# Kernel optimization log

Hardware: AMD Instinct MI355X
Metric: run time of the kernel (lower is better)

Reference implementation:

```python
import jax, jax.numpy as jnp
import numpy as np

N = 50000      # nodes
E = 1600000    # edges (avg degree 32)
F_IN = 256     # input feature dim
H = 128        # hidden == output size of GCN
C = 40         # num_class


def setup_inputs() -> dict:
    key = jax.random.key(0)
    ks = jax.random.split(key, 13)
    inp = {
        "features": jax.random.normal(ks[0], (N, F_IN), dtype=jnp.float32),
        "src": jax.random.randint(ks[1], (E,), 0, N, dtype=jnp.int32),
        "dst": jax.random.randint(ks[2], (E,), 0, N, dtype=jnp.int32),
        "edge_weight": jax.random.uniform(ks[3], (E,), dtype=jnp.float32),
        "y": jax.random.normal(ks[4], (N, C), dtype=jnp.float32),
        # GCN layer 1
        "W1": jax.random.normal(ks[5], (F_IN, H), dtype=jnp.float32) / np.sqrt(F_IN),
        "b1": jnp.zeros((H,), dtype=jnp.float32),
        # GCN layer 2
        "W2": jax.random.normal(ks[6], (H, H), dtype=jnp.float32) / np.sqrt(H),
        "b2": jnp.zeros((H,), dtype=jnp.float32),
        # y_fc_emb: Linear(num_class, output_size)
        "We": jax.random.normal(ks[7], (C, H), dtype=jnp.float32) / np.sqrt(C),
        "be": jnp.zeros((H,), dtype=jnp.float32),
        # y_fc: Linear(hidden*2, num_class)
        "Wf": jax.random.normal(ks[8], (2 * H, C), dtype=jnp.float32) / np.sqrt(2 * H),
        "bf": jnp.zeros((C,), dtype=jnp.float32),
    }
    return inp


def _spmm(edge_weight, src, dst, x, n):
    # (sparse adj) @ x : out[i] = sum_{(j->i)} w_ji * x[j]
    return jax.ops.segment_sum(edge_weight[:, None] * x[src], dst, num_segments=n)


def reference(features, src, dst, edge_weight, y, W1, b1, W2, b2, We, be, Wf, bf):
    n = features.shape[0]
    # F.normalize: L2 row-normalize with eps=1e-12 clamp
    norm = jnp.maximum(jnp.linalg.norm(features, axis=1, keepdims=True), 1e-12)
    x = features / norm
    # GCN layer 1: relu(adj @ (x @ W1) + b1)   (dropout = 0)
    h = jax.nn.relu(_spmm(edge_weight, src, dst, x @ W1, n) + b1)
    # GCN layer 2: adj @ (h @ W2) + b2
    h = _spmm(edge_weight, src, dst, h @ W2, n) + b2
    # label embedding + head
    y_emb = y @ We + be
    logits = jnp.concatenate([y_emb, h], axis=1) @ Wf + bf
    return jax.nn.softmax(logits, axis=-1)
```

## Files before the change

### kernel.cpp

```cpp
#include <hip/hip_runtime.h>
#include <hip/hip_bf16.h>
#include <hip/hip_fp16.h>
#include <cstdint>
#include <cstddef>
#include <cmath>

#define F_IN 256
#define HDIM 128
#define CCLS 40
#define NBMAX 1024
#define EPB_H 16384

typedef short bf16x8 __attribute__((ext_vector_type(8)));
typedef float f32x4 __attribute__((ext_vector_type(4)));

__device__ inline unsigned pkbf(float a, float b) {
  __hip_bfloat162 h = __float22bfloat162_rn(make_float2(a, b));
  unsigned u;
  __builtin_memcpy(&u, &h, 4);
  return u;
}
__device__ inline unsigned short bfr(float f) {
  __hip_bfloat16 h = __float2bfloat16(f);
  unsigned short u;
  __builtin_memcpy(&u, &h, 2);
  return u;
}
__device__ inline float f16tof(unsigned short hb) {
  __half hv;
  __builtin_memcpy(&hv, &hb, 2);
  return __half2float(hv);
}
__device__ inline unsigned short ftof16(float f) {
  __half hv = __float2half(f);
  unsigned short u;
  __builtin_memcpy(&u, &hv, 2);
  return u;
}

__global__ __launch_bounds__(256) void prep_kernel(const float* __restrict__ W1,
                                                   const float* __restrict__ W2,
                                                   unsigned short* __restrict__ W1T,
                                                   unsigned short* __restrict__ W2T,
                                                   const float* __restrict__ We,
                                                   const float* __restrict__ be,
                                                   const float* __restrict__ Wf,
                                                   const float* __restrict__ bf,
                                                   float* __restrict__ Wc,
                                                   float* __restrict__ bc,
                                                   const int* __restrict__ dst,
                                                   int* __restrict__ gcount,
                                                   int e, int nb) {
  const int b = blockIdx.x;
  const int t = threadIdx.x;
  if (b < 192) {
    int idx = b * 256 + t;
    if (idx < 128 * 256) {
      int nr = idx >> 8, k = idx & 255;
      W1T[idx] = bfr(W1[k * 128 + nr]);
    } else {
      int i2 = idx - 128 * 256;
      if (i2 < 128 * 128) {
        int nr = i2 >> 7, k = i2 & 127;
        W2T[i2] = bfr(W2[k * 128 + nr]);
      }
    }
  } else if (b < 194) {
    int part = b - 192;
    int lo = part * 800, hi = lo + 800;
    for (int i = lo + t; i < hi; i += 256) {
      int c = i / CCLS, j = i % CCLS;
      float s = 0.f;
      for (int f = 0; f < HDIM; ++f) s += We[c * HDIM + f] * Wf[f * CCLS + j];
      Wc[i] = s;
    }
    if (part == 0 && t < CCLS) {
      float s = bf[t];
      for (int f = 0; f < HDIM; ++f) s += be[f] * Wf[f * CCLS + t];
      bc[t] = s;
    }
  } else {
    __shared__ int h[NBMAX];
    for (int i = t; i < nb; i += 256) h[i] = 0;
    __syncthreads();
    int b4 = (b - 194) * (EPB_H / 4);
#pragma unroll
    for (int k = 0; k < EPB_H / 1024; ++k) {
      int gi = b4 + k * 256 + t;
      int e0 = gi * 4;
      int4 d = make_int4(-1, -1, -1, -1);
      if (e0 + 3 < e) d = ((const int4*)dst)[gi];
      else if (e0 < e) {
        d.x = dst[e0];
        if (e0 + 1 < e) d.y = dst[e0 + 1];
        if (e0 + 2 < e) d.z = dst[e0 + 2];
      }
      if (d.x >= 0) atomicAdd(&h[d.x >> 6], 1);
      if (d.y >= 0) atomicAdd(&h[d.y >> 6], 1);
      if (d.z >= 0) atomicAdd(&h[d.z >> 6], 1);
      if (d.w >= 0) atomicAdd(&h[d.w >> 6], 1);
    }
    __syncthreads();
    for (int i = t; i < nb; i += 256)
      if (h[i]) atomicAdd(&gcount[i], h[i]);
  }
}

#define EPB 8192
__global__ __launch_bounds__(256) void scatter_gemm1(const int* __restrict__ src,
                                                     const int* __restrict__ dst,
                                                     const float* __restrict__ w,
                                                     const int* __restrict__ gcount,
                                                     int* __restrict__ gcursor,
                                                     uint2* __restrict__ ews,
                                                     const float* __restrict__ X,
                                                     const unsigned short* __restrict__ WT,
                                                     unsigned short* __restrict__ C,
                                                     int e, int nb, int nsb, int M) {
  __shared__ char smem[64 * 264 * 2];
  const int t = threadIdx.x;
  if ((int)blockIdx.x < nsb) {
    int* hist = (int*)smem;
    int* sb   = hist + NBMAX;
    int* lcur = sb + NBMAX;
    int* part = lcur + NBMAX;
    for (int i = t; i < nb; i += 256) { hist[i] = 0; lcur[i] = 0; }
    __syncthreads();
    const int b4 = blockIdx.x * 2048;
    int4 dv[8];
#pragma unroll
    for (int k = 0; k < 8; ++k) {
      int gi = b4 + k * 256 + t;
      int e0 = gi * 4;
      int4 d = make_int4(-1, -1, -1, -1);
      if (e0 + 3 < e) d = ((const int4*)dst)[gi];
      else if (e0 < e) {
        d.x = dst[e0];
        if (e0 + 1 < e) d.y = dst[e0 + 1];
        if (e0 + 2 < e) d.z = dst[e0 + 2];
      }
      dv[k] = d;
      if (d.x >= 0) atomicAdd(&hist[d.x >> 6], 1);
      if (d.y >= 0) atomicAdd(&hist[d.y >> 6], 1);
      if (d.z >= 0) atomicAdd(&hist[d.z >> 6], 1);
      if (d.w >= 0) atomicAdd(&hist[d.w >> 6], 1);
    }
    __syncthreads();
    int v[4];
    int s = 0;
#pragma unroll
    for (int k = 0; k < 4; ++k) {
      int i = t * 4 + k;
      v[k] = (i < nb) ? gcount[i] : 0;
      s += v[k];
    }
    part[t] = s;
    __syncthreads();
    for (int off = 1; off < 256; off <<= 1) {
      int x = part[t];
      if (t >= off) x += part[t - off];
      __syncthreads();
      part[t] = x;
      __syncthreads();
    }
    int run = (t == 0) ? 0 : part[t - 1];
#pragma unroll
    for (int k = 0; k < 4; ++k) {
      int i = t * 4 + k;
      if (i < nb) sb[i] = run;
      run += v[k];
    }
    __syncthreads();
    for (int i = t; i < nb; i += 256) {
      int c = hist[i];
      sb[i] = sb[i] + (c ? atomicAdd(&gcursor[i], c) : 0);
    }
    __syncthreads();
#pragma unroll
    for (int k = 0; k < 8; ++k) {
      int gi = b4 + k * 256 + t;
      int e0 = gi * 4;
      if (e0 >= e) continue;
      int4 s4 = make_int4(0, 0, 0, 0);
      float4 w4 = make_float4(0.f, 0.f, 0.f, 0.f);
      if (e0 + 3 < e) { s4 = ((const int4*)src)[gi]; w4 = ((const float4*)w)[gi]; }
      else {
        s4.x = src[e0]; w4.x = w[e0];
        if (e0 + 1 < e) { s4.y = src[e0 + 1]; w4.y = w[e0 + 1]; }
        if (e0 + 2 < e) { s4.z = src[e0 + 2]; w4.z = w[e0 + 2]; }
      }
      int4 d = dv[k];
      if (d.x >= 0) { int bb = d.x >> 6; int r = atomicAdd(&lcur[bb], 1);
        ews[sb[bb] + r] = make_uint2(((unsigned)(d.x & 63) << 26) | (unsigned)s4.x, __float_as_uint(w4.x)); }
      if (d.y >= 0) { int bb = d.y >> 6; int r = atomicAdd(&lcur[bb], 1);
        ews[sb[bb] + r] = make_uint2(((unsigned)(d.y & 63) << 26) | (unsigned)s4.y, __float_as_uint(w4.y)); }
      if (d.z >= 0) { int bb = d.z >> 6; int r = atomicAdd(&lcur[bb], 1);
        ews[sb[bb] + r] = make_uint2(((unsigned)(d.z & 63) << 26) | (unsigned)s4.z, __float_as_uint(w4.z)); }
      if (d.w >= 0) { int bb = d.w >> 6; int r = atomicAdd(&lcur[bb], 1);
        ews[sb[bb] + r] = make_uint2(((unsigned)(d.w & 63) << 26) | (unsigned)s4.w, __float_as_uint(w4.w)); }
    }
  } else {
    unsigned short (*As)[264] = (unsigned short(*)[264])smem;
    const int w8 = t >> 6, l = t & 63;
    const int bm0 = (blockIdx.x - nsb) * 64;

    for (int rr = 0; rr < 16; ++rr) {
      int row = w8 * 16 + rr;
      int grow = bm0 + row;
      const float* p = X + (size_t)(grow < M ? grow : (M - 1)) * F_IN + l * 4;
      float4 v = *(const float4*)p;
      float s = v.x * v.x + v.y * v.y + v.z * v.z + v.w * v.w;
#pragma unroll
      for (int off = 32; off; off >>= 1) s += __shfl_xor(s, off, 64);
      float inv = 1.0f / fmaxf(sqrtf(s), 1e-12f);
      *(uint2*)&As[row][l * 4] =
          make_uint2(pkbf(v.x * inv, v.y * inv), pkbf(v.z * inv, v.w * inv));
    }

    const int ln = l & 15, quad = l >> 4;
    const int m0 = bm0 + w8 * 16;
    f32x4 acc[8];
#pragma unroll
    for (int i = 0; i < 8; ++i) acc[i] = (f32x4){0.f, 0.f, 0.f, 0.f};

#pragma unroll
    for (int k0 = 0; k0 < F_IN; k0 += 32) {
      bf16x8 af = *(const bf16x8*)&As[w8 * 16 + ln][k0 + quad * 8];
#pragma unroll
      for (int ti = 0; ti < 8; ++ti) {
        bf16x8 bfv = *(const bf16x8*)(WT + (size_t)(ti * 16 + ln) * F_IN + k0 + quad * 8);
        acc[ti] = __builtin_amdgcn_mfma_f32_16x16x32_bf16(af, bfv, acc[ti], 0, 0, 0);
      }
    }

#pragma unroll
    for (int r = 0; r < 4; ++r) {
      int grow = m0 + quad * 4 + r;
      if (grow < M) {
        unsigned short* cp = C + (size_t)grow * HDIM + ln;
#pragma unroll
        for (int ti = 0; ti < 8; ++ti) cp[ti * 16] = bfr(acc[ti][r]);
      }
    }
  }
}

__global__ __launch_bounds__(256) void bucket_sort(const uint2* __restrict__ ews,
                                                   const int* __restrict__ gcount,
                                                   unsigned* __restrict__ ews2,
                                                   int* __restrict__ row_off,
                                                   int n, int nb) {
  __shared__ int cnt64[64];
  __shared__ int cur[64];
  __shared__ int sred[4];
  const int t = threadIdx.x;
  const int b = blockIdx.x;
  int partial = 0;
  for (int i = t; i < b; i += 256) partial += gcount[i];
#pragma unroll
  for (int off = 32; off; off >>= 1) partial += __shfl_xor(partial, off, 64);
  if ((t & 63) == 0) sred[t >> 6] = partial;
  if (t < 64) cnt64[t] = 0;
  __syncthreads();
  const int e0 = sred[0] + sred[1] + sred[2] + sred[3];
  const int e1 = e0 + gcount[b];
  for (int i = e0 + t; i < e1; i += 256) atomicAdd(&cnt64[(unsigned)ews[i].x >> 26], 1);
  __syncthreads();
  if (t == 0) {
    int run = 0;
    for (int d = 0; d < 64; ++d) {
      int c = cnt64[d];
      cur[d] = run;
      run += c;
    }
  }
  __syncthreads();
  if (t < 64) {
    int node = b * 64 + t;
    if (node < n) row_off[node] = e0 + cur[t];
  }
  if (b == nb - 1 && t == 0) row_off[n] = e1;
  __syncthreads();
  for (int i = e0 + t; i < e1; i += 256) {
    uint2 p = ews[i];
    int d = (unsigned)p.x >> 26;
    int pos = e0 + atomicAdd(&cur[d], 1);
    unsigned rec = (p.x & 0xFFFFu) | ((unsigned)ftof16(__uint_as_float(p.y)) << 16);
    ews2[pos] = rec;
  }
}

#define SPMM_PAIR(ua, ub)                                                      \
  {                                                                            \
    unsigned u = half ? (ub) : (ua);                                           \
    float wt = f16tof((unsigned short)(u >> 16));                              \
    const uint2 xv = *(const uint2*)(xin + (size_t)(u & 0xFFFFu) * HDIM + fo); \
    acc.x = fmaf(wt, __uint_as_float(xv.x << 16), acc.x);                      \
    acc.y = fmaf(wt, __uint_as_float(xv.x & 0xFFFF0000u), acc.y);              \
    acc.z = fmaf(wt, __uint_as_float(xv.y << 16), acc.z);                      \
    acc.w = fmaf(wt, __uint_as_float(xv.y & 0xFFFF0000u), acc.w);              \
  }

template <int OUT_BF16>
__global__ __launch_bounds__(256) void spmm_bf16(const unsigned short* __restrict__ xin,
                                                 const unsigned* __restrict__ ews,
                                                 const int* __restrict__ row_off,
                                                 const float* __restrict__ bias,
                                                 void* __restrict__ outp, int n,
                                                 int do_relu) {
  const int t = threadIdx.x;
  const int l = t & 63;
  const int node = blockIdx.x * 4 + (t >> 6);
  if (node >= n) return;
  const int ue0 = __builtin_amdgcn_readfirstlane(row_off[node]);
  const int ue1 = __builtin_amdgcn_readfirstlane(row_off[node + 1]);
  const int cnt = ue1 - ue0;
  const unsigned* ep = ews + ue0;
  const int fo = (l & 31) * 4;
  const int half = l >> 5;
  float4 acc = make_float4(0.f, 0.f, 0.f, 0.f);

  int k = 0;
  for (; k + 16 <= cnt; k += 16) {
    unsigned a0 = ep[k + 0], a1 = ep[k + 1], a2 = ep[k + 2], a3 = ep[k + 3];
    unsigned a4 = ep[k + 4], a5 = ep[k + 5], a6 = ep[k + 6], a7 = ep[k + 7];
    unsigned a8 = ep[k + 8], a9 = ep[k + 9], a10 = ep[k + 10], a11 = ep[k + 11];
    unsigned a12 = ep[k + 12], a13 = ep[k + 13], a14 = ep[k + 14], a15 = ep[k + 15];
    SPMM_PAIR(a0, a1);
    SPMM_PAIR(a2, a3);
    SPMM_PAIR(a4, a5);
    SPMM_PAIR(a6, a7);
    SPMM_PAIR(a8, a9);
    SPMM_PAIR(a10, a11);
    SPMM_PAIR(a12, a13);
    SPMM_PAIR(a14, a15);
  }
  for (; k + 8 <= cnt; k += 8) {
    unsigned a0 = ep[k + 0], a1 = ep[k + 1], a2 = ep[k + 2], a3 = ep[k + 3];
    unsigned a4 = ep[k + 4], a5 = ep[k + 5], a6 = ep[k + 6], a7 = ep[k + 7];
    SPMM_PAIR(a0, a1);
    SPMM_PAIR(a2, a3);
    SPMM_PAIR(a4, a5);
    SPMM_PAIR(a6, a7);
  }
  for (; k < cnt; k += 2) {
    unsigned a0 = ep[k];
    unsigned a1 = (k + 1 < cnt) ? ep[k + 1] : 0u;
    SPMM_PAIR(a0, a1);
  }

  acc.x += __shfl_xor(acc.x, 32, 64);
  acc.y += __shfl_xor(acc.y, 32, 64);
  acc.z += __shfl_xor(acc.z, 32, 64);
  acc.w += __shfl_xor(acc.w, 32, 64);
  if (l < 32) {
    float4 bv = *(const float4*)(bias + fo);
    float4 r = make_float4(acc.x + bv.x, acc.y + bv.y, acc.z + bv.z, acc.w + bv.w);
    if (do_relu) {
      r.x = fmaxf(r.x, 0.f); r.y = fmaxf(r.y, 0.f);
      r.z = fmaxf(r.z, 0.f); r.w = fmaxf(r.w, 0.f);
    }
    if (OUT_BF16) {
      uint2 o = make_uint2(pkbf(r.x, r.y), pkbf(r.z, r.w));
      *(uint2*)((unsigned short*)outp + (size_t)node * HDIM + fo) = o;
    } else {
      *(float4*)((float*)outp + (size_t)node * HDIM + fo) = r;
    }
  }
}

template <int K>
__global__ __launch_bounds__(256) void gemm_mfma(const unsigned short* __restrict__ A,
                                                 const unsigned short* __restrict__ WT,
                                                 unsigned short* __restrict__ C, int M) {
  const int t = threadIdx.x;
  const int w = t >> 6, l = t & 63;
  const int ln = l & 15, quad = l >> 4;
  const int m0 = blockIdx.x * 64 + w * 16;
  const int arow = m0 + ln;
  const unsigned short* aptr = A + (size_t)(arow < M ? arow : (M - 1)) * K + quad * 8;

  f32x4 acc[8];
#pragma unroll
  for (int i = 0; i < 8; ++i) acc[i] = (f32x4){0.f, 0.f, 0.f, 0.f};

#pragma unroll
  for (int k0 = 0; k0 < K; k0 += 32) {
    bf16x8 af = *(const bf16x8*)(aptr + k0);
#pragma unroll
    for (int ti = 0; ti < 8; ++ti) {
      bf16x8 bfv = *(const bf16x8*)(WT + (size_t)(ti * 16 + ln) * K + k0 + quad * 8);
      acc[ti] = __builtin_amdgcn_mfma_f32_16x16x32_bf16(af, bfv, acc[ti], 0, 0, 0);
    }
  }

#pragma unroll
  for (int r = 0; r < 4; ++r) {
    int grow = m0 + quad * 4 + r;
    if (grow < M) {
      unsigned short* cp = C + (size_t)grow * HDIM + ln;
#pragma unroll
      for (int ti = 0; ti < 8; ++ti) cp[ti * 16] = bfr(acc[ti][r]);
    }
  }
}

__global__ __launch_bounds__(256) void head_kernel(const float* __restrict__ y,
                                                   const float* __restrict__ h2,
                                                   const float* __restrict__ Wc,
                                                   const float* __restrict__ bc,
                                                   const float* __restrict__ Wf,
                                                   float* __restrict__ out, int n) {
  __shared__ float sW[169 * CCLS];
  const int t = threadIdx.x;
  for (int i = t; i < 400; i += 256) ((float4*)sW)[i] = ((const float4*)Wc)[i];
  for (int i = t; i < 1280; i += 256)
    ((float4*)(sW + CCLS * CCLS))[i] = ((const float4*)(Wf + HDIM * CCLS))[i];
  if (t < 10) ((float4*)(sW + 168 * CCLS))[t] = ((const float4*)bc)[t];
  __syncthreads();

  const int node = blockIdx.x * 256 + t;
  const int nc = node < n ? node : n - 1;
  const float* zy = y + (size_t)nc * CCLS;
  const float* zh = h2 + (size_t)nc * HDIM;

  float acc[40];
#pragma unroll
  for (int cq = 0; cq < 10; ++cq) {
    float4 b4 = *(const float4*)&sW[168 * CCLS + cq * 4];
    acc[cq * 4 + 0] = b4.x; acc[cq * 4 + 1] = b4.y;
    acc[cq * 4 + 2] = b4.z; acc[cq * 4 + 3] = b4.w;
  }

#pragma unroll 2
  for (int kc = 0; kc < 10; ++kc) {
    float4 zv = *(const float4*)(zy + kc * 4);
    float zj[4] = {zv.x, zv.y, zv.z, zv.w};
#pragma unroll
    for (int j = 0; j < 4; ++j) {
      const float* wr = sW + (kc * 4 + j) * CCLS;
#pragma unroll
      for (int cq = 0; cq < 10; ++cq) {
        float4 w4 = *(const float4*)(wr + cq * 4);
        acc[cq * 4 + 0] = fmaf(zj[j], w4.x, acc[cq * 4 + 0]);
        acc[cq * 4 + 1] = fmaf(zj[j], w4.y, acc[cq * 4 + 1]);
        acc[cq * 4 + 2] = fmaf(zj[j], w4.z, acc[cq * 4 + 2]);
        acc[cq * 4 + 3] = fmaf(zj[j], w4.w, acc[cq * 4 + 3]);
      }
    }
  }
#pragma unroll 2
  for (int kc = 0; kc < 32; ++kc) {
    float4 zv = *(const float4*)(zh + kc * 4);
    float zj[4] = {zv.x, zv.y, zv.z, zv.w};
#pragma unroll
    for (int j = 0; j < 4; ++j) {
      const float* wr = sW + (40 + kc * 4 + j) * CCLS;
#pragma unroll
      for (int cq = 0; cq < 10; ++cq) {
        float4 w4 = *(const float4*)(wr + cq * 4);
        acc[cq * 4 + 0] = fmaf(zj[j], w4.x, acc[cq * 4 + 0]);
        acc[cq * 4 + 1] = fmaf(zj[j], w4.y, acc[cq * 4 + 1]);
        acc[cq * 4 + 2] = fmaf(zj[j], w4.z, acc[cq * 4 + 2]);
        acc[cq * 4 + 3] = fmaf(zj[j], w4.w, acc[cq * 4 + 3]);
      }
    }
  }

  float m = acc[0];
#pragma unroll
  for (int c = 1; c < 40; ++c) m = fmaxf(m, acc[c]);
  float sum = 0.f;
#pragma unroll
  for (int c = 0; c < 40; ++c) { acc[c] = __expf(acc[c] - m); sum += acc[c]; }
  float inv = 1.0f / sum;
  if (node < n) {
    float* op = out + (size_t)node * CCLS;
#pragma unroll
    for (int cq = 0; cq < 10; ++cq) {
      float4 o = make_float4(acc[cq * 4 + 0] * inv, acc[cq * 4 + 1] * inv,
                             acc[cq * 4 + 2] * inv, acc[cq * 4 + 3] * inv);
      *(float4*)(op + cq * 4) = o;
    }
  }
}

extern "C" void kernel_launch(void* const* d_in, const int* in_sizes, int n_in,
                              void* d_out, int out_size, void* d_ws, size_t ws_size,
                              hipStream_t stream) {
  (void)n_in; (void)out_size; (void)ws_size;
  const float* features = (const float*)d_in[0];
  const int*   src      = (const int*)d_in[1];
  const int*   dst      = (const int*)d_in[2];
  const float* ew       = (const float*)d_in[3];
  const float* y        = (const float*)d_in[4];
  const float* W1       = (const float*)d_in[5];
  const float* b1       = (const float*)d_in[6];
  const float* W2       = (const float*)d_in[7];
  const float* b2       = (const float*)d_in[8];
  const float* We       = (const float*)d_in[9];
  const float* be       = (const float*)d_in[10];
  const float* Wf       = (const float*)d_in[11];
  const float* bf       = (const float*)d_in[12];
  float* out = (float*)d_out;

  const int n = in_sizes[0] / F_IN;
  const int e = in_sizes[1];
  const int nb = (n + 63) >> 6;

  char* w = (char*)d_ws;
  auto take = [&](size_t bytes) {
    char* p = w;
    w += (bytes + 255) & ~(size_t)255;
    return p;
  };
  int*   gz       = (int*)take((size_t)2 * nb * 4);
  int*   gcount   = gz;
  int*   gcursor  = gz + nb;
  int*   row_off  = (int*)take((size_t)(n + 1) * 4);
  uint2* ews      = (uint2*)take((size_t)e * 8);
  unsigned* ews2  = (unsigned*)take((size_t)(e + 16) * 4);
  unsigned short* bufH1  = (unsigned short*)take((size_t)n * HDIM * 2);
  unsigned short* bufH2  = (unsigned short*)take((size_t)n * HDIM * 2);
  float* bufS     = (float*)take((size_t)n * HDIM * 4);
  unsigned short* W1T = (unsigned short*)take((size_t)HDIM * F_IN * 2);
  unsigned short* W2T = (unsigned short*)take((size_t)HDIM * HDIM * 2);
  float* Wc       = (float*)take(CCLS * CCLS * 4);
  float* bc       = (float*)take(CCLS * 4);

  const int hb = (e + EPB_H - 1) / EPB_H;
  const int nsb = (e + EPB - 1) / EPB;
  const int ngb = (n + 63) / 64;
  hipMemsetAsync(gz, 0, (size_t)2 * nb * 4, stream);
  prep_kernel<<<194 + hb, 256, 0, stream>>>(W1, W2, W1T, W2T, We, be, Wf, bf, Wc, bc,
                                            dst, gcount, e, nb);
  scatter_gemm1<<<nsb + ngb, 256, 0, stream>>>(src, dst, ew, gcount, gcursor, ews,
                                               features, W1T, bufH1, e, nb, nsb, n);
  bucket_sort<<<nb, 256, 0, stream>>>(ews, gcount, ews2, row_off, n, nb);

  spmm_bf16<1><<<(n + 3) / 4, 256, 0, stream>>>(bufH1, ews2, row_off, b1, bufH2, n, 1);
  gemm_mfma<HDIM><<<(n + 63) / 64, 256, 0, stream>>>(bufH2, W2T, bufH1, n);
  spmm_bf16<0><<<(n + 3) / 4, 256, 0, stream>>>(bufH1, ews2, row_off, b2, bufS, n, 0);
  head_kernel<<<(n + 255) / 256, 256, 0, stream>>>(y, bufS, Wc, bc, Wf, out, n);
}
```

Before: 343.8 us.

## Replace two-pass bucket sort with per-node counting and direct CSR scatter

The prep kernel now also counts edges per destination node with global atomics. A new row_scan kernel builds row offsets and per-node cursors from those counts. The scatter then writes packed fp16-weight records straight into their CSR slot using per-node global atomics. This removes the 8-byte intermediate edge buffer, the block-level histogram and scan in the scatter, and the separate bucket_sort pass. In exchange it adds millions of contended global atomics on a 50k-entry array and gives non-deterministic edge order within each row.

```diff
diff --git a/kernel.cpp b/kernel.cpp
--- a/kernel.cpp
+++ b/kernel.cpp
@@ -49,6 +49,7 @@
                                                    float* __restrict__ Wc,
                                                    float* __restrict__ bc,
                                                    const int* __restrict__ dst,
+                                                   int* __restrict__ ncnt,
                                                    int* __restrict__ gcount,
                                                    int e, int nb) {
   const int b = blockIdx.x;
@@ -95,112 +96,88 @@
         if (e0 + 1 < e) d.y = dst[e0 + 1];
         if (e0 + 2 < e) d.z = dst[e0 + 2];
       }
-      if (d.x >= 0) atomicAdd(&h[d.x >> 6], 1);
-      if (d.y >= 0) atomicAdd(&h[d.y >> 6], 1);
-      if (d.z >= 0) atomicAdd(&h[d.z >> 6], 1);
-      if (d.w >= 0) atomicAdd(&h[d.w >> 6], 1);
+      if (d.x >= 0) { atomicAdd(&h[d.x >> 6], 1); atomicAdd(&ncnt[d.x], 1); }
+      if (d.y >= 0) { atomicAdd(&h[d.y >> 6], 1); atomicAdd(&ncnt[d.y], 1); }
+      if (d.z >= 0) { atomicAdd(&h[d.z >> 6], 1); atomicAdd(&ncnt[d.z], 1); }
+      if (d.w >= 0) { atomicAdd(&h[d.w >> 6], 1); atomicAdd(&ncnt[d.w], 1); }
     }
     __syncthreads();
     for (int i = t; i < nb; i += 256)
       if (h[i]) atomicAdd(&gcount[i], h[i]);
   }
+}
+
+__global__ __launch_bounds__(256) void row_scan(const int* __restrict__ gcount,
+                                                const int* __restrict__ ncnt,
+                                                int* __restrict__ row_off,
+                                                int* __restrict__ cur,
+                                                int n, int nb, int e) {
+  __shared__ int sred[4];
+  const int t = threadIdx.x;
+  const int b = blockIdx.x;
+  int partial = 0;
+  for (int i = t; i < b; i += 256) partial += gcount[i];
+#pragma unroll
+  for (int off = 32; off; off >>= 1) partial += __shfl_xor(partial, off, 64);
+  if ((t & 63) == 0) sred[t >> 6] = partial;
+  __syncthreads();
+  const int e0 = sred[0] + sred[1] + sred[2] + sred[3];
+  if (t < 64) {
+    int node = b * 64 + t;
+    int c = (node < n) ? ncnt[node] : 0;
+    int x = c;
+#pragma unroll
+    for (int off = 1; off < 64; off <<= 1) {
+      int y = __shfl_up(x, off, 64);
+      if (t >= off) x += y;
+    }
+    int base = e0 + x - c;
+    if (node < n) { row_off[node] = base; cur[node] = base; }
+  }
+  if (b == nb - 1 && t == 0) row_off[n] = e;
 }
 
 #define EPB 8192
 __global__ __launch_bounds__(256) void scatter_gemm1(const int* __restrict__ src,
                                                      const int* __restrict__ dst,
                                                      const float* __restrict__ w,
-                                                     const int* __restrict__ gcount,
-                                                     int* __restrict__ gcursor,
-                                                     uint2* __restrict__ ews,
+                                                     int* __restrict__ cur,
+                                                     unsigned* __restrict__ ews2,
                                                      const float* __restrict__ X,
                                                      const unsigned short* __restrict__ WT,
                                                      unsigned short* __restrict__ C,
-                                                     int e, int nb, int nsb, int M) {
-  __shared__ char smem[64 * 264 * 2];
+                                                     int e, int nsb, int M) {
+  __shared__ unsigned short As[64][264];
   const int t = threadIdx.x;
   if ((int)blockIdx.x < nsb) {
-    int* hist = (int*)smem;
-    int* sb   = hist + NBMAX;
-    int* lcur = sb + NBMAX;
-    int* part = lcur + NBMAX;
-    for (int i = t; i < nb; i += 256) { hist[i] = 0; lcur[i] = 0; }
-    __syncthreads();
     const int b4 = blockIdx.x * 2048;
-    int4 dv[8];
-#pragma unroll
-    for (int k = 0; k < 8; ++k) {
-      int gi = b4 + k * 256 + t;
-      int e0 = gi * 4;
-      int4 d = make_int4(-1, -1, -1, -1);
-      if (e0 + 3 < e) d = ((const int4*)dst)[gi];
-      else if (e0 < e) {
-        d.x = dst[e0];
-        if (e0 + 1 < e) d.y = dst[e0 + 1];
-        if (e0 + 2 < e) d.z = dst[e0 + 2];
-      }
-      dv[k] = d;
-      if (d.x >= 0) atomicAdd(&hist[d.x >> 6], 1);
-      if (d.y >= 0) atomicAdd(&hist[d.y >> 6], 1);
-      if (d.z >= 0) atomicAdd(&hist[d.z >> 6], 1);
-      if (d.w >= 0) atomicAdd(&hist[d.w >> 6], 1);
-    }
-    __syncthreads();
-    int v[4];
-    int s = 0;
-#pragma unroll
-    for (int k = 0; k < 4; ++k) {
-      int i = t * 4 + k;
-      v[k] = (i < nb) ? gcount[i] : 0;
-      s += v[k];
-    }
-    part[t] = s;
-    __syncthreads();
-    for (int off = 1; off < 256; off <<= 1) {
-      int x = part[t];
-      if (t >= off) x += part[t - off];
-      __syncthreads();
-      part[t] = x;
-      __syncthreads();
-    }
-    int run = (t == 0) ? 0 : part[t - 1];
-#pragma unroll
-    for (int k = 0; k < 4; ++k) {
-      int i = t * 4 + k;
-      if (i < nb) sb[i] = run;
-      run += v[k];
-    }
-    __syncthreads();
-    for (int i = t; i < nb; i += 256) {
-      int c = hist[i];
-      sb[i] = sb[i] + (c ? atomicAdd(&gcursor[i], c) : 0);
-    }
-    __syncthreads();
 #pragma unroll
     for (int k = 0; k < 8; ++k) {
       int gi = b4 + k * 256 + t;
       int e0 = gi * 4;
       if (e0 >= e) continue;
+      int4 d = make_int4(-1, -1, -1, -1);
       int4 s4 = make_int4(0, 0, 0, 0);
       float4 w4 = make_float4(0.f, 0.f, 0.f, 0.f);
-      if (e0 + 3 < e) { s4 = ((const int4*)src)[gi]; w4 = ((const float4*)w)[gi]; }
-      else {
-        s4.x = src[e0]; w4.x = w[e0];
-        if (e0 + 1 < e) { s4.y = src[e0 + 1]; w4.y = w[e0 + 1]; }
-        if (e0 + 2 < e) { s4.z = src[e0 + 2]; w4.z = w[e0 + 2]; }
-      }
-      int4 d = dv[k];
-      if (d.x >= 0) { int bb = d.x >> 6; int r = atomicAdd(&lcur[bb], 1);
-        ews[sb[bb] + r] = make_uint2(((unsigned)(d.x & 63) << 26) | (unsigned)s4.x, __float_as_uint(w4.x)); }
-      if (d.y >= 0) { int bb = d.y >> 6; int r = atomicAdd(&lcur[bb], 1);
-        ews[sb[bb] + r] = make_uint2(((unsigned)(d.y & 63) << 26) | (unsigned)s4.y, __float_as_uint(w4.y)); }
-      if (d.z >= 0) { int bb = d.z >> 6; int r = atomicAdd(&lcur[bb], 1);
-        ews[sb[bb] + r] = make_uint2(((unsigned)(d.z & 63) << 26) | (unsigned)s4.z, __float_as_uint(w4.z)); }
-      if (d.w >= 0) { int bb = d.w >> 6; int r = atomicAdd(&lcur[bb], 1);
-        ews[sb[bb] + r] = make_uint2(((unsigned)(d.w & 63) << 26) | (unsigned)s4.w, __float_as_uint(w4.w)); }
+      if (e0 + 3 < e) {
+        d = ((const int4*)dst)[gi];
+        s4 = ((const int4*)src)[gi];
+        w4 = ((const float4*)w)[gi];
+      } else {
+        d.x = dst[e0]; s4.x = src[e0]; w4.x = w[e0];
+        if (e0 + 1 < e) { d.y = dst[e0 + 1]; s4.y = src[e0 + 1]; w4.y = w[e0 + 1]; }
+        if (e0 + 2 < e) { d.z = dst[e0 + 2]; s4.z = src[e0 + 2]; w4.z = w[e0 + 2]; }
+      }
+      if (d.x >= 0) { int p = atomicAdd(&cur[d.x], 1);
+        ews2[p] = ((unsigned)s4.x & 0xFFFFu) | ((unsigned)ftof16(w4.x) << 16); }
+      if (d.y >= 0) { int p = atomicAdd(&cur[d.y], 1);
+        ews2[p] = ((unsigned)s4.y & 0xFFFFu) | ((unsigned)ftof16(w4.y) << 16); }
+      if (d.z >= 0) { int p = atomicAdd(&cur[d.z], 1);
+        ews2[p] = ((unsigned)s4.z & 0xFFFFu) | ((unsigned)ftof16(w4.z) << 16); }
+      if (d.w >= 0) { int p = atomicAdd(&cur[d.w], 1);
+        ews2[p] = ((unsigned)s4.w & 0xFFFFu) | ((unsigned)ftof16(w4.w) << 16); }
     }
   } else {
-    unsigned short (*As)[264] = (unsigned short(*)[264])smem;
     const int w8 = t >> 6, l = t & 63;
     const int bm0 = (blockIdx.x - nsb) * 64;
 
@@ -242,51 +219,6 @@
         for (int ti = 0; ti < 8; ++ti) cp[ti * 16] = bfr(acc[ti][r]);
       }
     }
-  }
-}
-
-__global__ __launch_bounds__(256) void bucket_sort(const uint2* __restrict__ ews,
-                                                   const int* __restrict__ gcount,
-                                                   unsigned* __restrict__ ews2,
-                                                   int* __restrict__ row_off,
-                                                   int n, int nb) {
-  __shared__ int cnt64[64];
-  __shared__ int cur[64];
-  __shared__ int sred[4];
-  const int t = threadIdx.x;
-  const int b = blockIdx.x;
-  int partial = 0;
-  for (int i = t; i < b; i += 256) partial += gcount[i];
-#pragma unroll
-  for (int off = 32; off; off >>= 1) partial += __shfl_xor(partial, off, 64);
-  if ((t & 63) == 0) sred[t >> 6] = partial;
-  if (t < 64) cnt64[t] = 0;
-  __syncthreads();
-  const int e0 = sred[0] + sred[1] + sred[2] + sred[3];
-  const int e1 = e0 + gcount[b];
-  for (int i = e0 + t; i < e1; i += 256) atomicAdd(&cnt64[(unsigned)ews[i].x >> 26], 1);
-  __syncthreads();
-  if (t == 0) {
-    int run = 0;
-    for (int d = 0; d < 64; ++d) {
-      int c = cnt64[d];
-      cur[d] = run;
-      run += c;
-    }
-  }
-  __syncthreads();
-  if (t < 64) {
-    int node = b * 64 + t;
-    if (node < n) row_off[node] = e0 + cur[t];
-  }
-  if (b == nb - 1 && t == 0) row_off[n] = e1;
-  __syncthreads();
-  for (int i = e0 + t; i < e1; i += 256) {
-    uint2 p = ews[i];
-    int d = (unsigned)p.x >> 26;
-    int pos = e0 + atomicAdd(&cur[d], 1);
-    unsigned rec = (p.x & 0xFFFFu) | ((unsigned)ftof16(__uint_as_float(p.y)) << 16);
-    ews2[pos] = rec;
   }
 }
 
@@ -514,11 +446,11 @@
     w += (bytes + 255) & ~(size_t)255;
     return p;
   };
-  int*   gz       = (int*)take((size_t)2 * nb * 4);
-  int*   gcount   = gz;
-  int*   gcursor  = gz + nb;
+  int*   gz       = (int*)take((size_t)(n + nb) * 4);
+  int*   ncnt     = gz;
+  int*   gcount   = gz + n;
   int*   row_off  = (int*)take((size_t)(n + 1) * 4);
-  uint2* ews      = (uint2*)take((size_t)e * 8);
+  int*   cur      = (int*)take((size_t)n * 4);
   unsigned* ews2  = (unsigned*)take((size_t)(e + 16) * 4);
   unsigned short* bufH1  = (unsigned short*)take((size_t)n * HDIM * 2);
   unsigned short* bufH2  = (unsigned short*)take((size_t)n * HDIM * 2);
@@ -531,12 +463,12 @@
   const int hb = (e + EPB_H - 1) / EPB_H;
   const int nsb = (e + EPB - 1) / EPB;
   const int ngb = (n + 63) / 64;
-  hipMemsetAsync(gz, 0, (size_t)2 * nb * 4, stream);
+  hipMemsetAsync(gz, 0, (size_t)(n + nb) * 4, stream);
   prep_kernel<<<194 + hb, 256, 0, stream>>>(W1, W2, W1T, W2T, We, be, Wf, bf, Wc, bc,
-                                            dst, gcount, e, nb);
-  scatter_gemm1<<<nsb + ngb, 256, 0, stream>>>(src, dst, ew, gcount, gcursor, ews,
-                                               features, W1T, bufH1, e, nb, nsb, n);
-  bucket_sort<<<nb, 256, 0, stream>>>(ews, gcount, ews2, row_off, n, nb);
+                                            dst, ncnt, gcount, e, nb);
+  row_scan<<<nb, 256, 0, stream>>>(gcount, ncnt, row_off, cur, n, nb, e);
+  scatter_gemm1<<<nsb + ngb, 256, 0, stream>>>(src, dst, ew, cur, ews2,
+                                               features, W1T, bufH1, e, nsb, n);
 
   spmm_bf16<1><<<(n + 3) / 4, 256, 0, stream>>>(bufH1, ews2, row_off, b1, bufH2, n, 1);
   gemm_mfma<HDIM><<<(n + 63) / 64, 256, 0, stream>>>(bufH2, W2T, bufH1, n);
```

New measurement: 425.4 us. 23.7% more time.

## Rebalance preprocessing work across kernels and co-schedule gemm1 with bucket sort

Applied to the files above, without the earlier changes.

Splits the row-normalize + GEMM1 tiles so only the first 400 tiles run alongside the edge scatter, with the rest co-scheduled in the bucket-sort kernel. W2 transpose and the folded head weight computation also move from the prep kernel into that sort kernel. This balances load across the three launches and shortens the prep kernel. The sort itself now uses per-wave histograms and a wave-level scan instead of a serial single-thread prefix. The risk is that heterogeneous block types in one launch can leave a tail of slow blocks.

```diff
diff --git a/kernel.cpp b/kernel.cpp
--- a/kernel.cpp
+++ b/kernel.cpp
@@ -10,6 +10,7 @@
 #define CCLS 40
 #define NBMAX 1024
 #define EPB_H 16384
+#define EPB 8192
 
 typedef short bf16x8 __attribute__((ext_vector_type(8)));
 typedef float f32x4 __attribute__((ext_vector_type(4)));
@@ -38,52 +39,68 @@
   return u;
 }
 
+__device__ inline void gemm1_body(char* smem, int bm0, const float* __restrict__ X,
+                                  const unsigned short* __restrict__ WT,
+                                  unsigned short* __restrict__ C, int M, int t) {
+  unsigned short (*As)[264] = (unsigned short(*)[264])smem;
+  const int w8 = t >> 6, l = t & 63;
+
+  for (int rr = 0; rr < 16; ++rr) {
+    int row = w8 * 16 + rr;
+    int grow = bm0 + row;
+    const float* p = X + (size_t)(grow < M ? grow : (M - 1)) * F_IN + l * 4;
+    float4 v = *(const float4*)p;
+    float s = v.x * v.x + v.y * v.y + v.z * v.z + v.w * v.w;
+#pragma unroll
+    for (int off = 32; off; off >>= 1) s += __shfl_xor(s, off, 64);
+    float inv = 1.0f / fmaxf(sqrtf(s), 1e-12f);
+    *(uint2*)&As[row][l * 4] =
+        make_uint2(pkbf(v.x * inv, v.y * inv), pkbf(v.z * inv, v.w * inv));
+  }
+
+  const int ln = l & 15, quad = l >> 4;
+  const int m0 = bm0 + w8 * 16;
+  f32x4 acc[8];
+#pragma unroll
+  for (int i = 0; i < 8; ++i) acc[i] = (f32x4){0.f, 0.f, 0.f, 0.f};
+
+#pragma unroll
+  for (int k0 = 0; k0 < F_IN; k0 += 32) {
+    bf16x8 af = *(const bf16x8*)&As[w8 * 16 + ln][k0 + quad * 8];
+#pragma unroll
+    for (int ti = 0; ti < 8; ++ti) {
+      bf16x8 bfv = *(const bf16x8*)(WT + (size_t)(ti * 16 + ln) * F_IN + k0 + quad * 8);
+      acc[ti] = __builtin_amdgcn_mfma_f32_16x16x32_bf16(af, bfv, acc[ti], 0, 0, 0);
+    }
+  }
+
+#pragma unroll
+  for (int r = 0; r < 4; ++r) {
+    int grow = m0 + quad * 4 + r;
+    if (grow < M) {
+      unsigned short* cp = C + (size_t)grow * HDIM + ln;
+#pragma unroll
+      for (int ti = 0; ti < 8; ++ti) cp[ti * 16] = bfr(acc[ti][r]);
+    }
+  }
+}
+
 __global__ __launch_bounds__(256) void prep_kernel(const float* __restrict__ W1,
-                                                   const float* __restrict__ W2,
                                                    unsigned short* __restrict__ W1T,
-                                                   unsigned short* __restrict__ W2T,
-                                                   const float* __restrict__ We,
-                                                   const float* __restrict__ be,
-                                                   const float* __restrict__ Wf,
-                                                   const float* __restrict__ bf,
-                                                   float* __restrict__ Wc,
-                                                   float* __restrict__ bc,
                                                    const int* __restrict__ dst,
                                                    int* __restrict__ gcount,
                                                    int e, int nb) {
   const int b = blockIdx.x;
   const int t = threadIdx.x;
-  if (b < 192) {
+  if (b < 128) {
     int idx = b * 256 + t;
-    if (idx < 128 * 256) {
-      int nr = idx >> 8, k = idx & 255;
-      W1T[idx] = bfr(W1[k * 128 + nr]);
-    } else {
-      int i2 = idx - 128 * 256;
-      if (i2 < 128 * 128) {
-        int nr = i2 >> 7, k = i2 & 127;
-        W2T[i2] = bfr(W2[k * 128 + nr]);
-      }
-    }
-  } else if (b < 194) {
-    int part = b - 192;
-    int lo = part * 800, hi = lo + 800;
-    for (int i = lo + t; i < hi; i += 256) {
-      int c = i / CCLS, j = i % CCLS;
-      float s = 0.f;
-      for (int f = 0; f < HDIM; ++f) s += We[c * HDIM + f] * Wf[f * CCLS + j];
-      Wc[i] = s;
-    }
-    if (part == 0 && t < CCLS) {
-      float s = bf[t];
-      for (int f = 0; f < HDIM; ++f) s += be[f] * Wf[f * CCLS + t];
-      bc[t] = s;
-    }
+    int nr = idx >> 8, k = idx & 255;
+    W1T[idx] = bfr(W1[k * 128 + nr]);
   } else {
     __shared__ int h[NBMAX];
     for (int i = t; i < nb; i += 256) h[i] = 0;
     __syncthreads();
-    int b4 = (b - 194) * (EPB_H / 4);
+    int b4 = (b - 128) * (EPB_H / 4);
 #pragma unroll
     for (int k = 0; k < EPB_H / 1024; ++k) {
       int gi = b4 + k * 256 + t;
@@ -106,7 +123,6 @@
   }
 }
 
-#define EPB 8192
 __global__ __launch_bounds__(256) void scatter_gemm1(const int* __restrict__ src,
                                                      const int* __restrict__ dst,
                                                      const float* __restrict__ w,
@@ -200,93 +216,87 @@
         ews[sb[bb] + r] = make_uint2(((unsigned)(d.w & 63) << 26) | (unsigned)s4.w, __float_as_uint(w4.w)); }
     }
   } else {
-    unsigned short (*As)[264] = (unsigned short(*)[264])smem;
-    const int w8 = t >> 6, l = t & 63;
-    const int bm0 = (blockIdx.x - nsb) * 64;
-
-    for (int rr = 0; rr < 16; ++rr) {
-      int row = w8 * 16 + rr;
-      int grow = bm0 + row;
-      const float* p = X + (size_t)(grow < M ? grow : (M - 1)) * F_IN + l * 4;
-      float4 v = *(const float4*)p;
-      float s = v.x * v.x + v.y * v.y + v.z * v.z + v.w * v.w;
-#pragma unroll
-      for (int off = 32; off; off >>= 1) s += __shfl_xor(s, off, 64);
-      float inv = 1.0f / fmaxf(sqrtf(s), 1e-12f);
-      *(uint2*)&As[row][l * 4] =
-          make_uint2(pkbf(v.x * inv, v.y * inv), pkbf(v.z * inv, v.w * inv));
-    }
-
-    const int ln = l & 15, quad = l >> 4;
-    const int m0 = bm0 + w8 * 16;
-    f32x4 acc[8];
-#pragma unroll
-    for (int i = 0; i < 8; ++i) acc[i] = (f32x4){0.f, 0.f, 0.f, 0.f};
-
-#pragma unroll
-    for (int k0 = 0; k0 < F_IN; k0 += 32) {
-      bf16x8 af = *(const bf16x8*)&As[w8 * 16 + ln][k0 + quad * 8];
-#pragma unroll
-      for (int ti = 0; ti < 8; ++ti) {
-        bf16x8 bfv = *(const bf16x8*)(WT + (size_t)(ti * 16 + ln) * F_IN + k0 + quad * 8);
-        acc[ti] = __builtin_amdgcn_mfma_f32_16x16x32_bf16(af, bfv, acc[ti], 0, 0, 0);
-      }
-    }
-
-#pragma unroll
-    for (int r = 0; r < 4; ++r) {
-      int grow = m0 + quad * 4 + r;
-      if (grow < M) {
-        unsigned short* cp = C + (size_t)grow * HDIM + ln;
-#pragma unroll
-        for (int ti = 0; ti < 8; ++ti) cp[ti * 16] = bfr(acc[ti][r]);
-      }
-    }
-  }
-}
-
-__global__ __launch_bounds__(256) void bucket_sort(const uint2* __restrict__ ews,
-                                                   const int* __restrict__ gcount,
-                                                   unsigned* __restrict__ ews2,
-                                                   int* __restrict__ row_off,
-                                                   int n, int nb) {
-  __shared__ int cnt64[64];
-  __shared__ int cur[64];
-  __shared__ int sred[4];
+    gemm1_body(smem, (blockIdx.x - nsb) * 64, X, WT, C, M, t);
+  }
+}
+
+__global__ __launch_bounds__(256) void sort_misc(const uint2* __restrict__ ews,
+                                                 const int* __restrict__ gcount,
+                                                 unsigned* __restrict__ ews2,
+                                                 int* __restrict__ row_off,
+                                                 const float* __restrict__ X,
+                                                 const unsigned short* __restrict__ W1T,
+                                                 unsigned short* __restrict__ C,
+                                                 const float* __restrict__ W2,
+                                                 unsigned short* __restrict__ W2T,
+                                                 const float* __restrict__ We,
+                                                 const float* __restrict__ be,
+                                                 const float* __restrict__ Wf,
+                                                 const float* __restrict__ bf,
+                                                 float* __restrict__ Wc,
+                                                 float* __restrict__ bc,
+                                                 int n, int nb, int G1, int G2, int M) {
+  __shared__ char smem[64 * 264 * 2];
   const int t = threadIdx.x;
   const int b = blockIdx.x;
-  int partial = 0;
-  for (int i = t; i < b; i += 256) partial += gcount[i];
-#pragma unroll
-  for (int off = 32; off; off >>= 1) partial += __shfl_xor(partial, off, 64);
-  if ((t & 63) == 0) sred[t >> 6] = partial;
-  if (t < 64) cnt64[t] = 0;
-  __syncthreads();
-  const int e0 = sred[0] + sred[1] + sred[2] + sred[3];
-  const int e1 = e0 + gcount[b];
-  for (int i = e0 + t; i < e1; i += 256) atomicAdd(&cnt64[(unsigned)ews[i].x >> 26], 1);
-  __syncthreads();
-  if (t == 0) {
-    int run = 0;
-    for (int d = 0; d < 64; ++d) {
-      int c = cnt64[d];
-      cur[d] = run;
-      run += c;
-    }
-  }
-  __syncthreads();
-  if (t < 64) {
-    int node = b * 64 + t;
-    if (node < n) row_off[node] = e0 + cur[t];
-  }
-  if (b == nb - 1 && t == 0) row_off[n] = e1;
-  __syncthreads();
-  for (int i = e0 + t; i < e1; i += 256) {
-    uint2 p = ews[i];
-    int d = (unsigned)p.x >> 26;
-    int pos = e0 + atomicAdd(&cur[d], 1);
-    unsigned rec = (p.x & 0xFFFFu) | ((unsigned)ftof16(__uint_as_float(p.y)) << 16);
-    ews2[pos] = rec;
+  if (b < nb) {
+    int* cnt  = (int*)smem;
+    int* cur  = cnt + 256;
+    int* sred = cur + 64;
+    int partial = 0;
+    for (int i = t; i < b; i += 256) partial += gcount[i];
+#pragma unroll
+    for (int off = 32; off; off >>= 1) partial += __shfl_xor(partial, off, 64);
+    if ((t & 63) == 0) sred[t >> 6] = partial;
+    cnt[t] = 0;
+    __syncthreads();
+    const int e0 = sred[0] + sred[1] + sred[2] + sred[3];
+    const int e1 = e0 + gcount[b];
+    const int wv = t >> 6;
+    for (int i = e0 + t; i < e1; i += 256)
+      atomicAdd(&cnt[wv * 64 + ((unsigned)ews[i].x >> 26)], 1);
+    __syncthreads();
+    if (t < 64) {
+      int tot = cnt[t] + cnt[64 + t] + cnt[128 + t] + cnt[192 + t];
+      int x = tot;
+#pragma unroll
+      for (int off = 1; off < 64; off <<= 1) {
+        int y = __shfl_up(x, off, 64);
+        if (t >= off) x += y;
+      }
+      int excl = x - tot;
+      cur[t] = excl;
+      int node = b * 64 + t;
+      if (node < n) row_off[node] = e0 + excl;
+    }
+    if (b == nb - 1 && t == 0) row_off[n] = e1;
+    __syncthreads();
+    for (int i = e0 + t; i < e1; i += 256) {
+      uint2 p = ews[i];
+      int d = (unsigned)p.x >> 26;
+      int pos = e0 + atomicAdd(&cur[d], 1);
+      ews2[pos] = (p.x & 0xFFFFu) | ((unsigned)ftof16(__uint_as_float(p.y)) << 16);
+    }
+  } else if (b < nb + G2) {
+    gemm1_body(smem, (b - nb + G1) * 64, X, W1T, C, M, t);
+  } else if (b < nb + G2 + 64) {
+    int idx = (b - nb - G2) * 256 + t;
+    int nr = idx >> 7, k = idx & 127;
+    W2T[idx] = bfr(W2[k * 128 + nr]);
+  } else {
+    int part = b - (nb + G2 + 64);
+    int lo = part * 800, hi = lo + 800;
+    for (int i = lo + t; i < hi; i += 256) {
+      int c = i / CCLS, j = i % CCLS;
+      float s = 0.f;
+      for (int f = 0; f < HDIM; ++f) s += We[c * HDIM + f] * Wf[f * CCLS + j];
+      Wc[i] = s;
+    }
+    if (part == 0 && t < CCLS) {
+      float s = bf[t];
+      for (int f = 0; f < HDIM; ++f) s += be[f] * Wf[f * CCLS + t];
+      bc[t] = s;
+    }
   }
 }
 
@@ -528,15 +538,20 @@
   float* Wc       = (float*)take(CCLS * CCLS * 4);
   float* bc       = (float*)take(CCLS * 4);
 
-  const int hb = (e + EPB_H - 1) / EPB_H;
+  const int hb  = (e + EPB_H - 1) / EPB_H;
   const int nsb = (e + EPB - 1) / EPB;
   const int ngb = (n + 63) / 64;
+  const int G1  = ngb > 400 ? 400 : ngb;
+  const int G2  = ngb - G1;
+
   hipMemsetAsync(gz, 0, (size_t)2 * nb * 4, stream);
-  prep_kernel<<<194 + hb, 256, 0, stream>>>(W1, W2, W1T, W2T, We, be, Wf, bf, Wc, bc,
-                                            dst, gcount, e, nb);
-  scatter_gemm1<<<nsb + ngb, 256, 0, stream>>>(src, dst, ew, gcount, gcursor, ews,
-                                               features, W1T, bufH1, e, nb, nsb, n);
-  bucket_sort<<<nb, 256, 0, stream>>>(ews, gcount, ews2, row_off, n, nb);
+  prep_kernel<<<128 + hb, 256, 0, stream>>>(W1, W1T, dst, gcount, e, nb);
+  scatter_gemm1<<<nsb + G1, 256, 0, stream>>>(src, dst, ew, gcount, gcursor, ews,
+                                              features, W1T, bufH1, e, nb, nsb, n);
+  sort_misc<<<nb + G2 + 64 + 2, 256, 0, stream>>>(ews, gcount, ews2, row_off,
+                                                  features, W1T, bufH1,
+                                                  W2, W2T, We, be, Wf, bf, Wc, bc,
+                                                  n, nb, G1, G2, n);
 
   spmm_bf16<1><<<(n + 3) / 4, 256, 0, stream>>>(bufH1, ews2, row_off, b1, bufH2, n, 1);
   gemm_mfma<HDIM><<<(n + 63) / 64, 256, 0, stream>>>(bufH2, W2T, bufH1, n);
```

After: 367.3 us. +6.8%, slower.
